# Kernel tuning notes

Measured on AMD Instinct MI355X. Metric: run time of the kernel, lower is better.

## Reference

```python
import jax, jax.numpy as jnp
import numpy as np


def setup_inputs() -> dict:
    key = jax.random.key(0)
    k1, k2 = jax.random.split(key)
    x = jax.random.normal(k1, (16, 512, 64, 64), dtype=jnp.float32)
    beta = jax.random.uniform(k2, (1,), dtype=jnp.float32)
    return {"x": x, "beta": beta}


def reference(x, beta):
    b, c, h, w = x.shape
    hw = h * w
    # F.avg_pool2d(x, kernel_size=2, stride=2)
    Fp = x.reshape(b, c, h // 2, 2, w // 2, 2).mean(axis=(3, 5))  # [b,c,h/2,w/2]
    F_flat = Fp.reshape(b, c, -1)                                  # [b,c,hw/4]
    # channel-channel attention
    Sc = jax.nn.softmax(jnp.einsum('bcn,bdn->bcd', F_flat, F_flat), axis=-1)  # [b,c,c]
    Mc = jnp.einsum('bcd,bdn->bcn', Sc, F_flat).reshape(b, c, h // 2, w // 2)
    # bilinear upsample, align_corners=False (half-pixel convention)
    Mc = jax.image.resize(Mc, (b, c, h, w), method='bilinear')
    A_flat = x.reshape(b, c, hw)
    Mc_flat = Mc.reshape(b, c, hw)
    Ac = A_flat - A_flat.mean(axis=-1, keepdims=True)
    Mcc = Mc_flat - Mc_flat.mean(axis=-1, keepdims=True)
    cov = jnp.einsum('bcn,bdn->bcd', Ac, Mcc) / hw                # [b,c,c]
    Lc = Sc + cov
    Ec = jnp.einsum('bcd,bdn->bcn', Lc, A_flat).reshape(b, c, h, w)
    attention_map = beta[0] * Ec + x
    out = x * attention_map
    return (out, cov, Sc, Ec)
```

## Files before the change

### kernel.cpp

```cpp
#include <hip/hip_runtime.h>
#include <hip/hip_bf16.h>

typedef unsigned short u16;
typedef __attribute__((ext_vector_type(8))) short bf16x8;
typedef __attribute__((ext_vector_type(4))) float f32x4;

#define BB 16
#define CCH 512
#define HW 4096
#define PP 1024

__device__ __forceinline__ u16 f2bf(float f) {
  union { float f; unsigned u; } v; v.f = f;
  unsigned r = v.u + 0x7fffu + ((v.u >> 16) & 1u);
  return (u16)(r >> 16);
}
__device__ __forceinline__ float bf2f(u16 h) {
  union { unsigned u; float f; } v; v.u = ((unsigned)h) << 16;
  return v.f;
}

__global__ __launch_bounds__(256) void pool_kernel(
    const float* __restrict__ x, u16* __restrict__ Fb, u16* __restrict__ Xb,
    float* __restrict__ xmean) {
  int bc = blockIdx.x;
  const float2* xr = (const float2*)(x + (size_t)bc * HW);
  ushort2* xb2 = (ushort2*)(Xb + (size_t)bc * HW);
  u16* fb = Fb + (size_t)bc * PP;
  int t = threadIdx.x;
  float sum = 0.f;
#pragma unroll
  for (int s = 0; s < 4; ++s) {
    int p = t + s * 256;
    int py = p >> 5, px = p & 31;
    float2 a = xr[py * 64 + px];
    float2 b = xr[py * 64 + 32 + px];
    float pooled = 0.25f * (a.x + a.y + b.x + b.y);
    fb[p] = f2bf(pooled);
    sum += pooled;
    ushort2 ua; ua.x = f2bf(a.x); ua.y = f2bf(a.y);
    ushort2 ub; ub.x = f2bf(b.x); ub.y = f2bf(b.y);
    xb2[py * 64 + px] = ua;
    xb2[py * 64 + 32 + px] = ub;
  }
#pragma unroll
  for (int o = 32; o; o >>= 1) sum += __shfl_xor(sum, o);
  __shared__ float red[4];
  if ((t & 63) == 0) red[t >> 6] = sum;
  __syncthreads();
  if (t == 0) xmean[bc] = (red[0] + red[1] + red[2] + red[3]) * (1.0f / 1024.0f);
}

__global__ __launch_bounds__(256) void transpose_bf16(
    const u16* __restrict__ in, u16* __restrict__ out, int R, int C) {
  __shared__ u16 t[64][65];
  size_t bo = (size_t)blockIdx.z * R * C;
  int tr = blockIdx.y * 64, tc = blockIdx.x * 64;
  int tid = threadIdx.x;
#pragma unroll
  for (int s = 0; s < 2; ++s) {
    int i = tid + s * 256;
    int r = i >> 3, c8 = (i & 7) * 8;
    bf16x8 v = *(const bf16x8*)&in[bo + (size_t)(tr + r) * C + tc + c8];
#pragma unroll
    for (int j = 0; j < 8; ++j) t[r][c8 + j] = (u16)v[j];
  }
  __syncthreads();
#pragma unroll
  for (int s = 0; s < 2; ++s) {
    int i = tid + s * 256;
    int n = i >> 3, k8 = (i & 7) * 8;
    bf16x8 o;
#pragma unroll
    for (int j = 0; j < 8; ++j) o[j] = (short)t[k8 + j][n];
    *(bf16x8*)&out[bo + (size_t)(tc + n) * R + tr + k8] = o;
  }
}

__global__ void softmax_rows(float* __restrict__ G, u16* __restrict__ S1b) {
  size_t row = blockIdx.x;
  float* g = G + row * 512;
  int lane = threadIdx.x;
  float v[8];
  float mx = -3.4e38f;
#pragma unroll
  for (int i = 0; i < 8; ++i) { v[i] = g[lane + i * 64]; mx = fmaxf(mx, v[i]); }
#pragma unroll
  for (int o = 32; o; o >>= 1) mx = fmaxf(mx, __shfl_xor(mx, o));
  float s = 0.f;
#pragma unroll
  for (int i = 0; i < 8; ++i) { v[i] = expf(v[i] - mx); s += v[i]; }
#pragma unroll
  for (int o = 32; o; o >>= 1) s += __shfl_xor(s, o);
  float inv = 1.0f / s;
  int c = (int)(row & 511);
#pragma unroll
  for (int i = 0; i < 8; ++i) {
    int d = lane + i * 64;
    float sc = v[i] * inv;
    g[d] = sc;
    S1b[row * 512 + d] = f2bf(sc - (d == c ? 1.0f : 0.0f));
  }
}

__global__ __launch_bounds__(256) void upsample_kernel(
    const u16* __restrict__ Mcb, u16* __restrict__ Mup, float* __restrict__ mmean) {
  __shared__ float lm[1024];
  __shared__ float red[4];
  size_t bd = blockIdx.x;
  const u16* src = Mcb + bd * 1024;
  u16* dst = Mup + bd * 4096;
  int tid = threadIdx.x;
  for (int i = tid; i < 1024; i += 256) lm[i] = bf2f(src[i]);
  __syncthreads();
  float sum = 0.f;
#pragma unroll
  for (int it = 0; it < 16; ++it) {
    int idx = it * 256 + tid;
    int oy = idx >> 6, ox = idx & 63;
    int jy = oy >> 1, jx = ox >> 1;
    int y0, y1; float wy0;
    if (oy & 1) { y0 = jy; y1 = (jy < 31) ? jy + 1 : 31; wy0 = 0.75f; }
    else        { y0 = (jy > 0) ? jy - 1 : 0; y1 = jy; wy0 = (oy == 0) ? 0.0f : 0.25f; }
    int x0, x1; float wx0;
    if (ox & 1) { x0 = jx; x1 = (jx < 31) ? jx + 1 : 31; wx0 = 0.75f; }
    else        { x0 = (jx > 0) ? jx - 1 : 0; x1 = jx; wx0 = (ox == 0) ? 0.0f : 0.25f; }
    float wy1 = 1.0f - wy0, wx1 = 1.0f - wx0;
    float v = wy0 * (wx0 * lm[y0 * 32 + x0] + wx1 * lm[y0 * 32 + x1])
            + wy1 * (wx0 * lm[y1 * 32 + x0] + wx1 * lm[y1 * 32 + x1]);
    sum += v;
    dst[idx] = f2bf(v);
  }
#pragma unroll
  for (int o = 32; o; o >>= 1) sum += __shfl_xor(sum, o);
  if ((tid & 63) == 0) red[tid >> 6] = sum;
  __syncthreads();
  if (tid == 0) mmean[bd] = (red[0] + red[1] + red[2] + red[3]) * (1.0f / 4096.0f);
}

template <int MODE>
__global__ __launch_bounds__(256) void gemm_nt(
    const u16* __restrict__ A, const u16* __restrict__ B, int K, int lda, int ldb,
    size_t aStride, size_t bStride,
    float* __restrict__ outF, u16* __restrict__ outB,
    const u16* __restrict__ addB, const float* __restrict__ addF,
    const float* __restrict__ scp, const float* __restrict__ xm,
    const float* __restrict__ mm, int ldo, size_t oStride) {
  __shared__ u16 As[128 * 32];
  __shared__ u16 Bs[128 * 32];
  const int tid = threadIdx.x;
  const int lane = tid & 63, wave = tid >> 6;
  const int wr = wave >> 1, wc = wave & 1;
  const int z = blockIdx.z;
  const u16* Ab = A + (size_t)z * aStride + (size_t)(blockIdx.y * 128) * lda;
  const u16* Bb = B + (size_t)z * bStride + (size_t)(blockIdx.x * 128) * ldb;

  f32x4 acc[4][4] = {};

  const int r0 = tid >> 2;
  const int ko0 = (tid & 3) * 8;
  const int fr = lane & 15, kq = lane >> 4;

  for (int k0 = 0; k0 < K; k0 += 32) {
    __syncthreads();
#pragma unroll
    for (int s = 0; s < 2; ++s) {
      int row = r0 + s * 64;
      *(bf16x8*)&As[row * 32 + ko0] = *(const bf16x8*)&Ab[(size_t)row * lda + k0 + ko0];
      *(bf16x8*)&Bs[row * 32 + ko0] = *(const bf16x8*)&Bb[(size_t)row * ldb + k0 + ko0];
    }
    __syncthreads();
    bf16x8 af[4], bfr[4];
#pragma unroll
    for (int m = 0; m < 4; ++m)
      af[m] = *(const bf16x8*)&As[(wr * 64 + m * 16 + fr) * 32 + kq * 8];
#pragma unroll
    for (int n = 0; n < 4; ++n)
      bfr[n] = *(const bf16x8*)&Bs[(wc * 64 + n * 16 + fr) * 32 + kq * 8];
#pragma unroll
    for (int m = 0; m < 4; ++m)
#pragma unroll
      for (int n = 0; n < 4; ++n)
        acc[m][n] = __builtin_amdgcn_mfma_f32_16x16x32_bf16(af[m], bfr[n], acc[m][n], 0, 0, 0);
  }

  const int cq = lane >> 4, cr = lane & 15;
#pragma unroll
  for (int m = 0; m < 4; ++m) {
#pragma unroll
    for (int n = 0; n < 4; ++n) {
      int row0 = blockIdx.y * 128 + wr * 64 + m * 16 + cq * 4;
      int col  = blockIdx.x * 128 + wc * 64 + n * 16 + cr;
#pragma unroll
      for (int j = 0; j < 4; ++j) {
        int r = row0 + j;
        float val = acc[m][n][j];
        size_t idx = oStride * (size_t)z + (size_t)r * ldo + col;
        if constexpr (MODE == 0) {
          outF[idx] = val;
        } else if constexpr (MODE == 1) {
          outB[idx] = f2bf(val + bf2f(addB[idx]));
        } else if constexpr (MODE == 2) {
          float cv = val * (1.0f / 4096.0f) - xm[z * CCH + r] * mm[z * CCH + col];
          outF[idx] = cv;
          float l1 = scp[idx] + cv - (r == col ? 1.0f : 0.0f);
          outB[idx] = f2bf(l1);
        } else {
          outF[idx] = val + addF[idx];
        }
      }
    }
  }
}

__global__ void finalize_kernel(const float* __restrict__ x, const float* __restrict__ ec,
                                const float* __restrict__ beta, float* __restrict__ out) {
  float b = beta[0];
  size_t i = (size_t)blockIdx.x * 256 + threadIdx.x;
  size_t stride = (size_t)gridDim.x * 256;
  const float4* x4 = (const float4*)x;
  const float4* e4 = (const float4*)ec;
  float4* o4 = (float4*)out;
  size_t n4 = (size_t)BB * CCH * HW / 4;
  for (size_t p = i; p < n4; p += stride) {
    float4 xv = x4[p], ev = e4[p];
    float4 ov;
    ov.x = xv.x * (b * ev.x + xv.x);
    ov.y = xv.y * (b * ev.y + xv.y);
    ov.z = xv.z * (b * ev.z + xv.z);
    ov.w = xv.w * (b * ev.w + xv.w);
    o4[p] = ov;
  }
}

extern "C" void kernel_launch(void* const* d_in, const int* in_sizes, int n_in,
                              void* d_out, int out_size, void* d_ws, size_t ws_size,
                              hipStream_t stream) {
  const float* x = (const float*)d_in[0];
  const float* beta = (const float*)d_in[1];

  const size_t NX = (size_t)BB * CCH * HW;
  const size_t NCOV = (size_t)BB * CCH * CCH;

  float* out_f = (float*)d_out;
  float* cov_f = out_f + NX;
  float* sc_f  = cov_f + NCOV;
  float* ec_f  = sc_f + NCOV;

  u16* XbT = (u16*)d_out;
  u16* Mup = (u16*)d_out + NX;
  u16* Xb  = (u16*)ec_f;

  char* w = (char*)d_ws;
  u16* Fb   = (u16*)(w);
  u16* FbT  = (u16*)(w + 16777216);
  u16* Mcb  = (u16*)(w + 33554432);
  u16* S1b  = (u16*)(w + 50331648);
  u16* L1b  = (u16*)(w + 58720256);
  float* xmean = (float*)(w + 67108864);
  float* mmean = (float*)(w + 67141632);

  pool_kernel<<<BB * CCH, 256, 0, stream>>>(x, Fb, Xb, xmean);
  transpose_bf16<<<dim3(16, 8, BB), 256, 0, stream>>>(Fb, FbT, 512, 1024);
  transpose_bf16<<<dim3(64, 8, BB), 256, 0, stream>>>(Xb, XbT, 512, 4096);
  gemm_nt<0><<<dim3(4, 4, BB), 256, 0, stream>>>(
      Fb, Fb, 1024, 1024, 1024, (size_t)CCH * PP, (size_t)CCH * PP,
      sc_f, nullptr, nullptr, nullptr, nullptr, nullptr, nullptr, 512, NCOV / BB);
  softmax_rows<<<BB * CCH, 64, 0, stream>>>(sc_f, S1b);
  gemm_nt<1><<<dim3(8, 4, BB), 256, 0, stream>>>(
      S1b, FbT, 512, 512, 512, (size_t)CCH * CCH, (size_t)PP * CCH,
      nullptr, Mcb, Fb, nullptr, nullptr, nullptr, nullptr, 1024, (size_t)CCH * PP);
  upsample_kernel<<<BB * CCH, 256, 0, stream>>>(Mcb, Mup, mmean);
  gemm_nt<2><<<dim3(4, 4, BB), 256, 0, stream>>>(
      Xb, Mup, 4096, 4096, 4096, NX / BB, NX / BB,
      cov_f, L1b, nullptr, nullptr, sc_f, xmean, mmean, 512, NCOV / BB);
  gemm_nt<3><<<dim3(32, 4, BB), 256, 0, stream>>>(
      L1b, XbT, 512, 512, 512, (size_t)CCH * CCH, NX / BB,
      ec_f, nullptr, nullptr, x, nullptr, nullptr, nullptr, 4096, NX / BB);
  finalize_kernel<<<4096, 256, 0, stream>>>(x, ec_f, beta, out_f);
}
```

Before: 732.2 us.

## Split-K the Gram GEMMs, use direct global-to-LDS loads, fuse finalize into last GEMM

The F·F^T and X·Mup^T GEMMs use split-K (2 and 4 ways) to raise block count. Partial sums go to spare output memory and are reduced in softmax and in a new combine_cov kernel. GEMM tile staging now uses global_load_lds instead of register round-trips, and pool_kernel is vectorised to float4. When workspace allows, XbT moves to the workspace so the final GEMM can write both Ec and out, which removes the separate finalize pass. The cost is extra partial-sum traffic and a dependence on workspace size.

```diff
diff --git a/kernel.cpp b/kernel.cpp
--- a/kernel.cpp
+++ b/kernel.cpp
@@ -20,28 +20,36 @@
   return v.f;
 }
 
+typedef __attribute__((address_space(1))) const unsigned gas_u32;
+typedef __attribute__((address_space(3))) unsigned las_u32;
+__device__ __forceinline__ void gl_lds16(const u16* g, u16* l) {
+  __builtin_amdgcn_global_load_lds((gas_u32*)g, (las_u32*)l, 16, 0, 0);
+}
+
 __global__ __launch_bounds__(256) void pool_kernel(
     const float* __restrict__ x, u16* __restrict__ Fb, u16* __restrict__ Xb,
     float* __restrict__ xmean) {
   int bc = blockIdx.x;
-  const float2* xr = (const float2*)(x + (size_t)bc * HW);
-  ushort2* xb2 = (ushort2*)(Xb + (size_t)bc * HW);
-  u16* fb = Fb + (size_t)bc * PP;
+  const float4* xr4 = (const float4*)(x + (size_t)bc * HW);
+  ushort4* xb4 = (ushort4*)(Xb + (size_t)bc * HW);
+  ushort2* fb2 = (ushort2*)(Fb + (size_t)bc * PP);
   int t = threadIdx.x;
   float sum = 0.f;
 #pragma unroll
-  for (int s = 0; s < 4; ++s) {
-    int p = t + s * 256;
-    int py = p >> 5, px = p & 31;
-    float2 a = xr[py * 64 + px];
-    float2 b = xr[py * 64 + 32 + px];
-    float pooled = 0.25f * (a.x + a.y + b.x + b.y);
-    fb[p] = f2bf(pooled);
-    sum += pooled;
-    ushort2 ua; ua.x = f2bf(a.x); ua.y = f2bf(a.y);
-    ushort2 ub; ub.x = f2bf(b.x); ub.y = f2bf(b.y);
-    xb2[py * 64 + px] = ua;
-    xb2[py * 64 + 32 + px] = ub;
+  for (int s = 0; s < 2; ++s) {
+    int i = s * 256 + t;
+    int py = i >> 4, pxq = i & 15;
+    float4 a = xr4[(2 * py) * 16 + pxq];
+    float4 b = xr4[(2 * py + 1) * 16 + pxq];
+    float p0 = 0.25f * (a.x + a.y + b.x + b.y);
+    float p1 = 0.25f * (a.z + a.w + b.z + b.w);
+    ushort2 fp; fp.x = f2bf(p0); fp.y = f2bf(p1);
+    fb2[i] = fp;
+    sum += p0 + p1;
+    ushort4 ua; ua.x = f2bf(a.x); ua.y = f2bf(a.y); ua.z = f2bf(a.z); ua.w = f2bf(a.w);
+    ushort4 ub; ub.x = f2bf(b.x); ub.y = f2bf(b.y); ub.z = f2bf(b.z); ub.w = f2bf(b.w);
+    xb4[(2 * py) * 16 + pxq] = ua;
+    xb4[(2 * py + 1) * 16 + pxq] = ub;
   }
 #pragma unroll
   for (int o = 32; o; o >>= 1) sum += __shfl_xor(sum, o);
@@ -77,14 +85,22 @@
   }
 }
 
-__global__ void softmax_rows(float* __restrict__ G, u16* __restrict__ S1b) {
+__global__ void softmax_rows(const float* __restrict__ P, float* __restrict__ Sc,
+                             u16* __restrict__ S1b) {
   size_t row = blockIdx.x;
-  float* g = G + row * 512;
+  int z = (int)(row >> 9);
+  const float* p0 = P + ((size_t)z * 2) * 262144 + (size_t)(row & 511) * 512;
+  const float* p1 = p0 + 262144;
+  float* g = Sc + row * 512;
   int lane = threadIdx.x;
   float v[8];
   float mx = -3.4e38f;
 #pragma unroll
-  for (int i = 0; i < 8; ++i) { v[i] = g[lane + i * 64]; mx = fmaxf(mx, v[i]); }
+  for (int i = 0; i < 8; ++i) {
+    int d = lane + i * 64;
+    v[i] = p0[d] + p1[d];
+    mx = fmaxf(mx, v[i]);
+  }
 #pragma unroll
   for (int o = 32; o; o >>= 1) mx = fmaxf(mx, __shfl_xor(mx, o));
   float s = 0.f;
@@ -138,37 +154,40 @@
   if (tid == 0) mmean[bd] = (red[0] + red[1] + red[2] + red[3]) * (1.0f / 4096.0f);
 }
 
-template <int MODE>
+template <int MODE, int LOGSPLIT>
 __global__ __launch_bounds__(256) void gemm_nt(
     const u16* __restrict__ A, const u16* __restrict__ B, int K, int lda, int ldb,
     size_t aStride, size_t bStride,
-    float* __restrict__ outF, u16* __restrict__ outB,
+    float* __restrict__ outF, float* __restrict__ out2F, u16* __restrict__ outB,
     const u16* __restrict__ addB, const float* __restrict__ addF,
-    const float* __restrict__ scp, const float* __restrict__ xm,
-    const float* __restrict__ mm, int ldo, size_t oStride) {
+    const float* __restrict__ bp, int ldo, size_t oStride) {
   __shared__ u16 As[128 * 32];
   __shared__ u16 Bs[128 * 32];
   const int tid = threadIdx.x;
   const int lane = tid & 63, wave = tid >> 6;
   const int wr = wave >> 1, wc = wave & 1;
-  const int z = blockIdx.z;
-  const u16* Ab = A + (size_t)z * aStride + (size_t)(blockIdx.y * 128) * lda;
-  const u16* Bb = B + (size_t)z * bStride + (size_t)(blockIdx.x * 128) * ldb;
+  const int zi = blockIdx.z;
+  const int sp = zi & ((1 << LOGSPLIT) - 1);
+  const int z = zi >> LOGSPLIT;
+  const u16* Ab = A + (size_t)z * aStride + (size_t)sp * K + (size_t)(blockIdx.y * 128) * lda;
+  const u16* Bb = B + (size_t)z * bStride + (size_t)sp * K + (size_t)(blockIdx.x * 128) * ldb;
 
   f32x4 acc[4][4] = {};
 
-  const int r0 = tid >> 2;
-  const int ko0 = (tid & 3) * 8;
+  const int stRow = lane >> 2;
+  const int stCol = (lane & 3) * 8;
+  u16* aL0 = As + (wave * 16) * 32;
+  u16* aL1 = As + ((wave + 4) * 16) * 32;
+  u16* bL0 = Bs + (wave * 16) * 32;
+  u16* bL1 = Bs + ((wave + 4) * 16) * 32;
   const int fr = lane & 15, kq = lane >> 4;
 
   for (int k0 = 0; k0 < K; k0 += 32) {
     __syncthreads();
-#pragma unroll
-    for (int s = 0; s < 2; ++s) {
-      int row = r0 + s * 64;
-      *(bf16x8*)&As[row * 32 + ko0] = *(const bf16x8*)&Ab[(size_t)row * lda + k0 + ko0];
-      *(bf16x8*)&Bs[row * 32 + ko0] = *(const bf16x8*)&Bb[(size_t)row * ldb + k0 + ko0];
-    }
+    gl_lds16(Ab + (size_t)(wave * 16 + stRow) * lda + k0 + stCol, aL0);
+    gl_lds16(Ab + (size_t)((wave + 4) * 16 + stRow) * lda + k0 + stCol, aL1);
+    gl_lds16(Bb + (size_t)(wave * 16 + stRow) * ldb + k0 + stCol, bL0);
+    gl_lds16(Bb + (size_t)((wave + 4) * 16 + stRow) * ldb + k0 + stCol, bL1);
     __syncthreads();
     bf16x8 af[4], bfr[4];
 #pragma unroll
@@ -184,6 +203,8 @@
         acc[m][n] = __builtin_amdgcn_mfma_f32_16x16x32_bf16(af[m], bfr[n], acc[m][n], 0, 0, 0);
   }
 
+  float betaV = 0.f;
+  if constexpr (MODE == 4) betaV = bp[0];
   const int cq = lane >> 4, cr = lane & 15;
 #pragma unroll
   for (int m = 0; m < 4; ++m) {
@@ -195,21 +216,41 @@
       for (int j = 0; j < 4; ++j) {
         int r = row0 + j;
         float val = acc[m][n][j];
-        size_t idx = oStride * (size_t)z + (size_t)r * ldo + col;
+        size_t idx = oStride * (size_t)zi + (size_t)r * ldo + col;
         if constexpr (MODE == 0) {
           outF[idx] = val;
         } else if constexpr (MODE == 1) {
           outB[idx] = f2bf(val + bf2f(addB[idx]));
-        } else if constexpr (MODE == 2) {
-          float cv = val * (1.0f / 4096.0f) - xm[z * CCH + r] * mm[z * CCH + col];
-          outF[idx] = cv;
-          float l1 = scp[idx] + cv - (r == col ? 1.0f : 0.0f);
-          outB[idx] = f2bf(l1);
-        } else {
+        } else if constexpr (MODE == 3) {
           outF[idx] = val + addF[idx];
+        } else if constexpr (MODE == 4) {
+          float xv = addF[idx];
+          float ec = val + xv;
+          outF[idx] = ec;
+          out2F[idx] = xv * (betaV * ec + xv);
         }
       }
     }
+  }
+}
+
+__global__ __launch_bounds__(256) void combine_cov(
+    const float* __restrict__ parts, const float* __restrict__ sc,
+    const float* __restrict__ xm, const float* __restrict__ mm,
+    float* __restrict__ cov, u16* __restrict__ L1b) {
+  int row = blockIdx.x;
+  int z = row >> 9, r = row & 511;
+  size_t base = (size_t)z * 262144 + (size_t)r * 512;
+  size_t pz = (size_t)z * 4 * 262144 + (size_t)r * 512;
+  float xmr = xm[row];
+#pragma unroll
+  for (int j = 0; j < 2; ++j) {
+    int c = threadIdx.x + j * 256;
+    float s = parts[pz + c] + parts[pz + 262144 + c] +
+              parts[pz + 2 * 262144 + c] + parts[pz + 3 * 262144 + c];
+    float cv = s * (1.0f / 4096.0f) - xmr * mm[z * 512 + c];
+    cov[base + c] = cv;
+    L1b[base + c] = f2bf(sc[base + c] + cv - (r == c ? 1.0f : 0.0f));
   }
 }
 
@@ -247,9 +288,8 @@
   float* sc_f  = cov_f + NCOV;
   float* ec_f  = sc_f + NCOV;
 
-  u16* XbT = (u16*)d_out;
-  u16* Mup = (u16*)d_out + NX;
-  u16* Xb  = (u16*)ec_f;
+  u16* Xb = (u16*)ec_f;
+  float* spare = ec_f + NX / 2;
 
   char* w = (char*)d_ws;
   u16* Fb   = (u16*)(w);
@@ -259,23 +299,35 @@
   u16* L1b  = (u16*)(w + 58720256);
   float* xmean = (float*)(w + 67108864);
   float* mmean = (float*)(w + 67141632);
+  const size_t WS_BASE = 67174400;
+  const bool bigws = ws_size >= WS_BASE + (size_t)134217728;
+
+  u16* XbT = bigws ? (u16*)(w + WS_BASE) : (u16*)d_out;
+  u16* Mup = (u16*)d_out + NX;
 
   pool_kernel<<<BB * CCH, 256, 0, stream>>>(x, Fb, Xb, xmean);
   transpose_bf16<<<dim3(16, 8, BB), 256, 0, stream>>>(Fb, FbT, 512, 1024);
   transpose_bf16<<<dim3(64, 8, BB), 256, 0, stream>>>(Xb, XbT, 512, 4096);
-  gemm_nt<0><<<dim3(4, 4, BB), 256, 0, stream>>>(
-      Fb, Fb, 1024, 1024, 1024, (size_t)CCH * PP, (size_t)CCH * PP,
-      sc_f, nullptr, nullptr, nullptr, nullptr, nullptr, nullptr, 512, NCOV / BB);
-  softmax_rows<<<BB * CCH, 64, 0, stream>>>(sc_f, S1b);
-  gemm_nt<1><<<dim3(8, 4, BB), 256, 0, stream>>>(
+  gemm_nt<0, 1><<<dim3(4, 4, BB * 2), 256, 0, stream>>>(
+      Fb, Fb, 512, 1024, 1024, (size_t)CCH * PP, (size_t)CCH * PP,
+      spare, nullptr, nullptr, nullptr, nullptr, nullptr, 512, 262144);
+  softmax_rows<<<BB * CCH, 64, 0, stream>>>(spare, sc_f, S1b);
+  gemm_nt<1, 0><<<dim3(8, 4, BB), 256, 0, stream>>>(
       S1b, FbT, 512, 512, 512, (size_t)CCH * CCH, (size_t)PP * CCH,
-      nullptr, Mcb, Fb, nullptr, nullptr, nullptr, nullptr, 1024, (size_t)CCH * PP);
+      nullptr, nullptr, Mcb, Fb, nullptr, nullptr, 1024, (size_t)CCH * PP);
   upsample_kernel<<<BB * CCH, 256, 0, stream>>>(Mcb, Mup, mmean);
-  gemm_nt<2><<<dim3(4, 4, BB), 256, 0, stream>>>(
-      Xb, Mup, 4096, 4096, 4096, NX / BB, NX / BB,
-      cov_f, L1b, nullptr, nullptr, sc_f, xmean, mmean, 512, NCOV / BB);
-  gemm_nt<3><<<dim3(32, 4, BB), 256, 0, stream>>>(
-      L1b, XbT, 512, 512, 512, (size_t)CCH * CCH, NX / BB,
-      ec_f, nullptr, nullptr, x, nullptr, nullptr, nullptr, 4096, NX / BB);
-  finalize_kernel<<<4096, 256, 0, stream>>>(x, ec_f, beta, out_f);
-}
+  gemm_nt<0, 2><<<dim3(4, 4, BB * 4), 256, 0, stream>>>(
+      Xb, Mup, 1024, 4096, 4096, NX / BB, NX / BB,
+      spare, nullptr, nullptr, nullptr, nullptr, nullptr, 512, 262144);
+  combine_cov<<<BB * CCH, 256, 0, stream>>>(spare, sc_f, xmean, mmean, cov_f, L1b);
+  if (bigws) {
+    gemm_nt<4, 0><<<dim3(32, 4, BB), 256, 0, stream>>>(
+        L1b, XbT, 512, 512, 512, (size_t)CCH * CCH, NX / BB,
+        ec_f, out_f, nullptr, nullptr, x, beta, 4096, NX / BB);
+  } else {
+    gemm_nt<3, 0><<<dim3(32, 4, BB), 256, 0, stream>>>(
+        L1b, XbT, 512, 512, 512, (size_t)CCH * CCH, NX / BB,
+        ec_f, nullptr, nullptr, nullptr, x, nullptr, 4096, NX / BB);
+    finalize_kernel<<<4096, 256, 0, stream>>>(x, ec_f, beta, out_f);
+  }
+}
```

Measured after the change: 698.4 us. -4.6%, faster.
